# Performance work log

Hardware: AMD Instinct MI355X
Metric: run time of the kernel (lower is better)

The kernel has to match this reference:

```python
import jax, jax.numpy as jnp
import numpy as np

I1, H1, H2, NC = 38, 50, 15, 14

def _lstm(x, w_ih, w_hh, b_ih, b_hh):
    # x: [B, T, I]; weights in torch layout: w_ih [4H, I], w_hh [4H, H]
    # torch gate order: i, f, g, o
    B, T, _ = x.shape
    H = w_hh.shape[1]
    gx = jnp.einsum('bti,gi->btg', x, w_ih) + b_ih + b_hh  # [B, T, 4H]
    gx = jnp.swapaxes(gx, 0, 1)  # [T, B, 4H]

    def step(carry, g_t):
        h, c = carry
        g = g_t + h @ w_hh.T
        i_g, f_g, c_g, o_g = jnp.split(g, 4, axis=-1)
        i_g = jax.nn.sigmoid(i_g)
        f_g = jax.nn.sigmoid(f_g)
        o_g = jax.nn.sigmoid(o_g)
        c = f_g * c + i_g * jnp.tanh(c_g)
        h = o_g * jnp.tanh(c)
        return (h, c), h

    init = (jnp.zeros((B, H), x.dtype), jnp.zeros((B, H), x.dtype))
    _, hs = jax.lax.scan(step, init, gx)  # hs: [T, B, H]
    return jnp.swapaxes(hs, 0, 1)  # [B, T, H]

def setup_inputs() -> dict:
    key = jax.random.key(0)
    ks = jax.random.split(key, 12)
    s1 = 1.0 / np.sqrt(H1)
    s2 = 1.0 / np.sqrt(H2)
    u = lambda k, shape, s: jax.random.uniform(k, shape, jnp.float32, -s, s)
    return {
        'x': jax.random.normal(ks[0], (4096, 256, I1), jnp.float32),
        'w_ih1': u(ks[1], (4 * H1, I1), s1),
        'w_hh1': u(ks[2], (4 * H1, H1), s1),
        'b_ih1': u(ks[3], (4 * H1,), s1),
        'b_hh1': u(ks[4], (4 * H1,), s1),
        'w_ih2': u(ks[5], (4 * H2, H1), s2),
        'w_hh2': u(ks[6], (4 * H2, H2), s2),
        'b_ih2': u(ks[7], (4 * H2,), s2),
        'b_hh2': u(ks[8], (4 * H2,), s2),
        'w_fc': u(ks[9], (NC, H2), s2),
        'b_fc': u(ks[10], (NC,), s2),
    }

def reference(x, w_ih1, w_hh1, b_ih1, b_hh1, w_ih2, w_hh2, b_ih2, b_hh2, w_fc, b_fc):
    out = _lstm(x, w_ih1, w_hh1, b_ih1, b_hh1)          # [B, T, 50]
    # dropout(0.2) is identity in eval mode
    out = _lstm(out, w_ih2, w_hh2, b_ih2, b_hh2)        # [B, T, 15]
    return out[:, -1, :] @ w_fc.T + b_fc                # [B, 14]
```

## Files before the change

kernel.cpp:

```cpp
#include <hip/hip_runtime.h>


typedef _Float16 f16x8 __attribute__((ext_vector_type(8)));
typedef float    f32x4 __attribute__((ext_vector_type(4)));

#if __has_builtin(__builtin_amdgcn_exp2f)
#define DEV_EXP2(x) __builtin_amdgcn_exp2f(x)
#else
#define DEV_EXP2(x) exp2f(x)
#endif
#if __has_builtin(__builtin_amdgcn_rcpf)
#define DEV_RCP(x) __builtin_amdgcn_rcpf(x)
#else
#define DEV_RCP(x) (1.0f/(x))
#endif

#define I1 38
#define H1 50
#define H2 15
#define NC 14
#define TT 256
#define SB 16
#define XS 136
#define NTH 512
#define L2E 2.885390081777927f
#define L1E 1.442695040888963f

#define MF(A,B,C) __builtin_amdgcn_mfma_f32_16x16x32_f16((A),(B),(C),0,0,0)

__device__ __forceinline__ float sigm(float v)  { return DEV_RCP(1.f + DEV_EXP2(-L1E * v)); }
__device__ __forceinline__ float tanh_f(float v){ return 1.f - 2.f * DEV_RCP(1.f + DEV_EXP2(L2E * v)); }

__launch_bounds__(NTH, 1)
__global__ void lstm2_fused(const float* __restrict__ x,
                            const float* __restrict__ w_ih1, const float* __restrict__ w_hh1,
                            const float* __restrict__ b_ih1, const float* __restrict__ b_hh1,
                            const float* __restrict__ w_ih2, const float* __restrict__ w_hh2,
                            const float* __restrict__ b_ih2, const float* __restrict__ b_hh2,
                            const float* __restrict__ w_fc, const float* __restrict__ b_fc,
                            float* __restrict__ out)
{
  __shared__ __align__(16) _Float16 bufA[2][SB][XS];

  const int tid  = threadIdx.x;
  const int wv   = tid >> 6;
  const int lane = tid & 63;
  const int lm   = lane & 15;
  const int lk   = lane >> 4;
  const int blk  = blockIdx.x;
  const float* xblk = x + (size_t)blk * SB * TT * I1;

  for (int i = tid; i < 2*SB*XS; i += NTH) ((_Float16*)bufA)[i] = (_Float16)0.f;

  auto welem = [&](bool il1, bool valid, int u, int g, int k) -> _Float16 {
    float w = 0.f;
    if (valid) {
      if (il1) {
        if (k < I1)                w = w_ih1[(g*H1 + u)*I1 + k];
        else if (k < I1 + H1)      w = w_hh1[(g*H1 + u)*H1 + (k - I1)];
      } else {
        if (k >= I1 && k < I1+H1)             w = w_ih2[(g*H2 + u)*H1 + (k - I1)];
        else if (k >= I1+H1 && k < I1+H1+H2)  w = w_hh2[(g*H2 + u)*H2 + (k - I1 - H1)];
      }
    }
    return (_Float16)w;
  };

  const int t1 = wv + 8;
  const int r0 = wv*16 + lm, u0f = r0 >> 2, g0 = r0 & 3;
  const int r1 = t1*16 + lm, q1 = r1 >> 2, g1 = r1 & 3;
  const bool il1f = (q1 < H1);
  const int  u1f = il1f ? q1 : (q1 - H1);
  const bool w16 = (wv == 0);
  const bool c16 = w16 && (lm < 4);

  f16x8 W0[3], W1[4], W16[3];
  #pragma unroll
  for (int ks = 0; ks < 3; ++ks) {
    f16x8 v;
    #pragma unroll
    for (int e = 0; e < 8; ++e) v[e] = welem(true, true, u0f, g0, ks*32 + lk*8 + e);
    W0[ks] = v;
  }
  #pragma unroll
  for (int ks = 0; ks < 4; ++ks) {
    f16x8 v;
    #pragma unroll
    for (int e = 0; e < 8; ++e) v[e] = welem(il1f, true, u1f, g1, ks*32 + lk*8 + e);
    W1[ks] = v;
  }
  #pragma unroll
  for (int j = 0; j < 3; ++j) {
    f16x8 v;
    #pragma unroll
    for (int e = 0; e < 8; ++e) v[e] = welem(false, c16, 14, lm & 3, (j+1)*32 + lk*8 + e);
    W16[j] = v;
  }

  const int uS0 = 4*wv + lk;
  const int d0  = 38 + uS0;
  const int uS1 = 32 + 4*wv + lk;
  const bool il1u = (uS1 < H1);
  const int  uS1r = il1u ? uS1 : (uS1 - H1);
  const int  d1   = il1u ? (38 + uS1) : (88 + uS1r);
  const bool hasC = w16 && (lk == 0);

  float sb0[4], sb1[4], sbC[4];
  #pragma unroll
  for (int m = 0; m < 4; ++m) {
    sb0[m] = b_ih1[m*H1 + uS0] + b_hh1[m*H1 + uS0];
    sb1[m] = il1u ? (b_ih1[m*H1 + uS1] + b_hh1[m*H1 + uS1])
                  : (b_ih2[m*H2 + uS1r] + b_hh2[m*H2 + uS1r]);
    sbC[m] = b_ih2[m*H2 + 14] + b_hh2[m*H2 + 14];
  }

  const int e1x = tid + 512;
  const bool v1 = (tid < SB*I1 - 512);
  const int s0 = tid / I1,  k0 = tid % I1;
  const int s1 = e1x / I1,  k1 = e1x % I1;
  const int gb0 = s0*TT*I1 + k0, gb1 = v1 ? (s1*TT*I1 + k1) : 0;
  const int lb0 = s0*XS + k0,    lb1 = v1 ? (s1*XS + k1) : 0;

  __syncthreads();
  {
    _Float16* b0 = &bufA[0][0][0];
    b0[lb0] = (_Float16)xblk[gb0];
    if (v1) b0[lb1] = (_Float16)xblk[gb1];
  }
  float xA0 = 0.f, xA1 = 0.f, xB0 = 0.f, xB1 = 0.f;
  xA0 = xblk[gb0 + I1];
  if (v1) xA1 = xblk[gb1 + I1];
  __syncthreads();

  float cS0 = 0.f, cS1 = 0.f, cC = 0.f;

#define STEP(T, XC0, XC1, XN0, XN1) do {                                        \
    _Float16* cur = &bufA[(T) & 1][0][0];                                       \
    _Float16* nxt = &bufA[((T) & 1) ^ 1][0][0];                                 \
    if ((T) + 2 < TT) {                                                         \
      const int go = ((T) + 2) * I1;                                            \
      XN0 = xblk[gb0 + go];                                                     \
      if (v1) XN1 = xblk[gb1 + go];                                             \
    }                                                                           \
    f16x8 a0 = *(const f16x8*)(cur + lm*XS +      lk*8);                        \
    f16x8 a1 = *(const f16x8*)(cur + lm*XS + 32 + lk*8);                        \
    f16x8 a2 = *(const f16x8*)(cur + lm*XS + 64 + lk*8);                        \
    f16x8 a3 = *(const f16x8*)(cur + lm*XS + 96 + lk*8);                        \
    {                                                                           \
      f32x4 acc = (f32x4){sb0[0], sb0[1], sb0[2], sb0[3]};                      \
      acc = MF(W0[0], a0, acc);                                                 \
      acc = MF(W0[1], a1, acc);                                                 \
      acc = MF(W0[2], a2, acc);                                                 \
      if ((T) < TT) {                                                           \
        float ig = sigm(acc[0]), fg = sigm(acc[1]);                             \
        float gg = tanh_f(acc[2]), og = sigm(acc[3]);                           \
        cS0 = fg*cS0 + ig*gg;                                                   \
        nxt[lm*XS + d0] = (_Float16)(og * tanh_f(cS0));                         \
      }                                                                         \
    }                                                                           \
    {                                                                           \
      f32x4 acc = (f32x4){sb1[0], sb1[1], sb1[2], sb1[3]};                      \
      acc = MF(W1[0], a0, acc);                                                 \
      acc = MF(W1[1], a1, acc);                                                 \
      acc = MF(W1[2], a2, acc);                                                 \
      acc = MF(W1[3], a3, acc);                                                 \
      const bool up = il1u ? ((T) < TT) : ((T) >= 1);                           \
      if (up) {                                                                 \
        float ig = sigm(acc[0]), fg = sigm(acc[1]);                             \
        float gg = tanh_f(acc[2]), og = sigm(acc[3]);                           \
        cS1 = fg*cS1 + ig*gg;                                                   \
        nxt[lm*XS + d1] = (_Float16)(og * tanh_f(cS1));                         \
      }                                                                         \
    }                                                                           \
    if (w16) {                                                                  \
      f32x4 acc = (f32x4){sbC[0], sbC[1], sbC[2], sbC[3]};                      \
      acc = MF(W16[0], a1, acc);                                                \
      acc = MF(W16[1], a2, acc);                                                \
      acc = MF(W16[2], a3, acc);                                                \
      if (hasC && (T) >= 1) {                                                   \
        float ig = sigm(acc[0]), fg = sigm(acc[1]);                             \
        float gg = tanh_f(acc[2]), og = sigm(acc[3]);                           \
        cC = fg*cC + ig*gg;                                                     \
        nxt[lm*XS + 102] = (_Float16)(og * tanh_f(cC));                         \
      }                                                                         \
    }                                                                           \
    if ((T) + 1 < TT) {                                                         \
      nxt[lb0] = (_Float16)XC0;                                                 \
      if (v1) nxt[lb1] = (_Float16)XC1;                                         \
    }                                                                           \
    __syncthreads();                                                            \
  } while (0)

  int t = 0;
  for (;;) {
    STEP(t, xA0, xA1, xB0, xB1);
    if (++t > TT) break;
    STEP(t, xB0, xB1, xA0, xA1);
    if (++t > TT) break;
  }
#undef STEP

  if (tid < SB*NC) {
    int s = tid / NC, n = tid % NC;
    float acc = b_fc[n];
    #pragma unroll
    for (int u = 0; u < H2; ++u)
      acc += (float)bufA[1][s][88 + u] * w_fc[n*H2 + u];
    out[((size_t)blk*SB + s)*NC + n] = acc;
  }
}

extern "C" void kernel_launch(void* const* d_in, const int* in_sizes, int n_in,
                              void* d_out, int out_size, void* d_ws, size_t ws_size,
                              hipStream_t stream) {
  (void)n_in; (void)d_ws; (void)ws_size; (void)out_size;
  const float* x     = (const float*)d_in[0];
  const float* w_ih1 = (const float*)d_in[1];
  const float* w_hh1 = (const float*)d_in[2];
  const float* b_ih1 = (const float*)d_in[3];
  const float* b_hh1 = (const float*)d_in[4];
  const float* w_ih2 = (const float*)d_in[5];
  const float* w_hh2 = (const float*)d_in[6];
  const float* b_ih2 = (const float*)d_in[7];
  const float* b_hh2 = (const float*)d_in[8];
  const float* w_fc  = (const float*)d_in[9];
  const float* b_fc  = (const float*)d_in[10];
  float* out = (float*)d_out;

  const int B = in_sizes[0] / (TT * I1);
  dim3 grid(B / SB), block(NTH);
  lstm2_fused<<<grid, block, 0, stream>>>(x, w_ih1, w_hh1, b_ih1, b_hh1,
                                          w_ih2, w_hh2, b_ih2, b_hh2,
                                          w_fc, b_fc, out);
}
```

Before: 163.3 us.

## Stage input timesteps through double-buffered LDS windows with vectorized loads

Replaces the per-step scalar global loads of x, which were prefetched two steps ahead into registers, with float4 loads of 8-timestep windows per sample. The windows are converted to fp16 and staged in a double-buffered shared-memory array. Each step then copies its x slice from LDS into the recurrent input buffer. This cuts the number of global load instructions and makes the accesses coalesced. The trade-off is that the global load latency now lands inside one step out of every eight, and the kernel uses extra shared memory.

```diff
diff --git a/kernel.cpp b/kernel.cpp
--- a/kernel.cpp
+++ b/kernel.cpp
@@ -2,6 +2,7 @@
 
 
 typedef _Float16 f16x8 __attribute__((ext_vector_type(8)));
+typedef _Float16 f16x4 __attribute__((ext_vector_type(4)));
 typedef float    f32x4 __attribute__((ext_vector_type(4)));
 
 #if __has_builtin(__builtin_amdgcn_exp2f)
@@ -23,6 +24,7 @@
 #define SB 16
 #define XS 136
 #define NTH 512
+#define WROW 304
 #define L2E 2.885390081777927f
 #define L1E 1.442695040888963f
 
@@ -41,6 +43,7 @@
                             float* __restrict__ out)
 {
   __shared__ __align__(16) _Float16 bufA[2][SB][XS];
+  __shared__ __align__(16) _Float16 s_win[2][SB][WROW];
 
   const int tid  = threadIdx.x;
   const int wv   = tid >> 6;
@@ -114,91 +117,98 @@
     sbC[m] = b_ih2[m*H2 + 14] + b_hh2[m*H2 + 14];
   }
 
+  auto load_window = [&](int t0, int buf) {
+    #pragma unroll
+    for (int it = 0; it < 3; ++it) {
+      int c = it*NTH + tid;
+      if (c < SB*76) {
+        int s = c / 76, r = c % 76;
+        const float4 v = *(const float4*)(xblk + (size_t)s*(TT*I1) + t0*I1 + 4*r);
+        f16x4 h;
+        h[0] = (_Float16)v.x; h[1] = (_Float16)v.y;
+        h[2] = (_Float16)v.z; h[3] = (_Float16)v.w;
+        *(f16x4*)&s_win[buf][s][4*r] = h;
+      }
+    }
+  };
+
   const int e1x = tid + 512;
   const bool v1 = (tid < SB*I1 - 512);
   const int s0 = tid / I1,  k0 = tid % I1;
   const int s1 = e1x / I1,  k1 = e1x % I1;
-  const int gb0 = s0*TT*I1 + k0, gb1 = v1 ? (s1*TT*I1 + k1) : 0;
-  const int lb0 = s0*XS + k0,    lb1 = v1 ? (s1*XS + k1) : 0;
-
+  const int lb0 = s0*XS + k0, lb1 = v1 ? (s1*XS + k1) : 0;
+
+  load_window(0, 0);
+  load_window(8, 1);
   __syncthreads();
   {
     _Float16* b0 = &bufA[0][0][0];
-    b0[lb0] = (_Float16)xblk[gb0];
-    if (v1) b0[lb1] = (_Float16)xblk[gb1];
-  }
-  float xA0 = 0.f, xA1 = 0.f, xB0 = 0.f, xB1 = 0.f;
-  xA0 = xblk[gb0 + I1];
-  if (v1) xA1 = xblk[gb1 + I1];
+    b0[lb0] = s_win[0][s0][k0];
+    if (v1) b0[lb1] = s_win[0][s1][k1];
+  }
   __syncthreads();
 
   float cS0 = 0.f, cS1 = 0.f, cC = 0.f;
 
-#define STEP(T, XC0, XC1, XN0, XN1) do {                                        \
-    _Float16* cur = &bufA[(T) & 1][0][0];                                       \
-    _Float16* nxt = &bufA[((T) & 1) ^ 1][0][0];                                 \
-    if ((T) + 2 < TT) {                                                         \
-      const int go = ((T) + 2) * I1;                                            \
-      XN0 = xblk[gb0 + go];                                                     \
-      if (v1) XN1 = xblk[gb1 + go];                                             \
-    }                                                                           \
-    f16x8 a0 = *(const f16x8*)(cur + lm*XS +      lk*8);                        \
-    f16x8 a1 = *(const f16x8*)(cur + lm*XS + 32 + lk*8);                        \
-    f16x8 a2 = *(const f16x8*)(cur + lm*XS + 64 + lk*8);                        \
-    f16x8 a3 = *(const f16x8*)(cur + lm*XS + 96 + lk*8);                        \
-    {                                                                           \
-      f32x4 acc = (f32x4){sb0[0], sb0[1], sb0[2], sb0[3]};                      \
-      acc = MF(W0[0], a0, acc);                                                 \
-      acc = MF(W0[1], a1, acc);                                                 \
-      acc = MF(W0[2], a2, acc);                                                 \
-      if ((T) < TT) {                                                           \
-        float ig = sigm(acc[0]), fg = sigm(acc[1]);                             \
-        float gg = tanh_f(acc[2]), og = sigm(acc[3]);                           \
-        cS0 = fg*cS0 + ig*gg;                                                   \
-        nxt[lm*XS + d0] = (_Float16)(og * tanh_f(cS0));                         \
-      }                                                                         \
-    }                                                                           \
-    {                                                                           \
-      f32x4 acc = (f32x4){sb1[0], sb1[1], sb1[2], sb1[3]};                      \
-      acc = MF(W1[0], a0, acc);                                                 \
-      acc = MF(W1[1], a1, acc);                                                 \
-      acc = MF(W1[2], a2, acc);                                                 \
-      acc = MF(W1[3], a3, acc);                                                 \
-      const bool up = il1u ? ((T) < TT) : ((T) >= 1);                           \
-      if (up) {                                                                 \
-        float ig = sigm(acc[0]), fg = sigm(acc[1]);                             \
-        float gg = tanh_f(acc[2]), og = sigm(acc[3]);                           \
-        cS1 = fg*cS1 + ig*gg;                                                   \
-        nxt[lm*XS + d1] = (_Float16)(og * tanh_f(cS1));                         \
-      }                                                                         \
-    }                                                                           \
-    if (w16) {                                                                  \
-      f32x4 acc = (f32x4){sbC[0], sbC[1], sbC[2], sbC[3]};                      \
-      acc = MF(W16[0], a1, acc);                                                \
-      acc = MF(W16[1], a2, acc);                                                \
-      acc = MF(W16[2], a3, acc);                                                \
-      if (hasC && (T) >= 1) {                                                   \
-        float ig = sigm(acc[0]), fg = sigm(acc[1]);                             \
-        float gg = tanh_f(acc[2]), og = sigm(acc[3]);                           \
-        cC = fg*cC + ig*gg;                                                     \
-        nxt[lm*XS + 102] = (_Float16)(og * tanh_f(cC));                         \
-      }                                                                         \
-    }                                                                           \
-    if ((T) + 1 < TT) {                                                         \
-      nxt[lb0] = (_Float16)XC0;                                                 \
-      if (v1) nxt[lb1] = (_Float16)XC1;                                         \
-    }                                                                           \
-    __syncthreads();                                                            \
-  } while (0)
-
-  int t = 0;
-  for (;;) {
-    STEP(t, xA0, xA1, xB0, xB1);
-    if (++t > TT) break;
-    STEP(t, xB0, xB1, xA0, xA1);
-    if (++t > TT) break;
-  }
-#undef STEP
+  for (int t = 0; t <= TT; ++t) {
+    _Float16* cur = &bufA[t & 1][0][0];
+    _Float16* nxt = &bufA[(t & 1) ^ 1][0][0];
+
+    if ((t & 7) == 7 && t + 9 < TT)
+      load_window(t + 9, ((t + 9) >> 3) & 1);
+
+    f16x8 a0 = *(const f16x8*)(cur + lm*XS +      lk*8);
+    f16x8 a1 = *(const f16x8*)(cur + lm*XS + 32 + lk*8);
+    f16x8 a2 = *(const f16x8*)(cur + lm*XS + 64 + lk*8);
+    f16x8 a3 = *(const f16x8*)(cur + lm*XS + 96 + lk*8);
+
+    {
+      f32x4 acc = (f32x4){sb0[0], sb0[1], sb0[2], sb0[3]};
+      acc = MF(W0[0], a0, acc);
+      acc = MF(W0[1], a1, acc);
+      acc = MF(W0[2], a2, acc);
+      if (t < TT) {
+        float ig = sigm(acc[0]), fg = sigm(acc[1]);
+        float gg = tanh_f(acc[2]), og = sigm(acc[3]);
+        cS0 = fg*cS0 + ig*gg;
+        nxt[lm*XS + d0] = (_Float16)(og * tanh_f(cS0));
+      }
+    }
+    {
+      f32x4 acc = (f32x4){sb1[0], sb1[1], sb1[2], sb1[3]};
+      acc = MF(W1[0], a0, acc);
+      acc = MF(W1[1], a1, acc);
+      acc = MF(W1[2], a2, acc);
+      acc = MF(W1[3], a3, acc);
+      const bool up = il1u ? (t < TT) : (t >= 1);
+      if (up) {
+        float ig = sigm(acc[0]), fg = sigm(acc[1]);
+        float gg = tanh_f(acc[2]), og = sigm(acc[3]);
+        cS1 = fg*cS1 + ig*gg;
+        nxt[lm*XS + d1] = (_Float16)(og * tanh_f(cS1));
+      }
+    }
+    if (w16) {
+      f32x4 acc = (f32x4){sbC[0], sbC[1], sbC[2], sbC[3]};
+      acc = MF(W16[0], a1, acc);
+      acc = MF(W16[1], a2, acc);
+      acc = MF(W16[2], a3, acc);
+      if (hasC && t >= 1) {
+        float ig = sigm(acc[0]), fg = sigm(acc[1]);
+        float gg = tanh_f(acc[2]), og = sigm(acc[3]);
+        cC = fg*cC + ig*gg;
+        nxt[lm*XS + 102] = (_Float16)(og * tanh_f(cC));
+      }
+    }
+
+    if (t + 1 < TT) {
+      const int tw = (t + 1) & 7, bw = ((t + 1) >> 3) & 1;
+      nxt[lb0] = s_win[bw][s0][tw*I1 + k0];
+      if (v1) nxt[lb1] = s_win[bw][s1][tw*I1 + k1];
+    }
+
+    __syncthreads();
+  }
 
   if (tid < SB*NC) {
     int s = tid / NC, n = tid % NC;
```

After: 201.8 us. +23.5%, slower.

## Halve sequences per block and fold gate tiles onto four waves

Applied to the files above, without the earlier changes.

Each block now handles 8 sequences with 256 threads instead of 16 with 512. Each of the four waves runs four gate tiles rather than two, and MFMA rows 8-15 duplicate rows 0-7 with their writes masked off. With launch bounds of 2 blocks per CU there are twice as many blocks, which shortens per-step barrier cost and should raise occupancy. In exchange, half of the MFMA work is wasted on duplicated rows and each wave holds more weight registers, which may cap how many waves fit.

```diff
diff --git a/kernel.cpp b/kernel.cpp
--- a/kernel.cpp
+++ b/kernel.cpp
@@ -20,9 +20,9 @@
 #define H2 15
 #define NC 14
 #define TT 256
-#define SB 16
+#define SB 8
 #define XS 136
-#define NTH 512
+#define NTH 256
 #define L2E 2.885390081777927f
 #define L1E 1.442695040888963f
 
@@ -31,7 +31,7 @@
 __device__ __forceinline__ float sigm(float v)  { return DEV_RCP(1.f + DEV_EXP2(-L1E * v)); }
 __device__ __forceinline__ float tanh_f(float v){ return 1.f - 2.f * DEV_RCP(1.f + DEV_EXP2(L2E * v)); }
 
-__launch_bounds__(NTH, 1)
+__launch_bounds__(NTH, 2)
 __global__ void lstm2_fused(const float* __restrict__ x,
                             const float* __restrict__ w_ih1, const float* __restrict__ w_hh1,
                             const float* __restrict__ b_ih1, const float* __restrict__ b_hh1,
@@ -47,6 +47,7 @@
   const int lane = tid & 63;
   const int lm   = lane & 15;
   const int lk   = lane >> 4;
+  const int arow = lm & 7;
   const int blk  = blockIdx.x;
   const float* xblk = x + (size_t)blk * SB * TT * I1;
 
@@ -66,28 +67,37 @@
     return (_Float16)w;
   };
 
-  const int t1 = wv + 8;
-  const int r0 = wv*16 + lm, u0f = r0 >> 2, g0 = r0 & 3;
-  const int r1 = t1*16 + lm, q1 = r1 >> 2, g1 = r1 & 3;
-  const bool il1f = (q1 < H1);
-  const int  u1f = il1f ? q1 : (q1 - H1);
-  const bool w16 = (wv == 0);
+  int   uF[4]; bool il1F[4];
+  #pragma unroll
+  for (int s = 0; s < 4; ++s) {
+    const int r = (wv + 4*s)*16 + lm;
+    const int q = r >> 2;
+    il1F[s] = (q < H1);
+    uF[s]   = il1F[s] ? q : (q - H1);
+  }
+  const int gF = lm & 3;
+  const bool w16 = (wv == 3);
   const bool c16 = w16 && (lm < 4);
 
-  f16x8 W0[3], W1[4], W16[3];
+  f16x8 W0[3], W1[3], W2[3], W3[4], W16[3];
   #pragma unroll
   for (int ks = 0; ks < 3; ++ks) {
-    f16x8 v;
-    #pragma unroll
-    for (int e = 0; e < 8; ++e) v[e] = welem(true, true, u0f, g0, ks*32 + lk*8 + e);
-    W0[ks] = v;
+    f16x8 v0, v1v, v2;
+    #pragma unroll
+    for (int e = 0; e < 8; ++e) {
+      const int k = ks*32 + lk*8 + e;
+      v0[e]  = welem(il1F[0], true, uF[0], gF, k);
+      v1v[e] = welem(il1F[1], true, uF[1], gF, k);
+      v2[e]  = welem(il1F[2], true, uF[2], gF, k);
+    }
+    W0[ks] = v0; W1[ks] = v1v; W2[ks] = v2;
   }
   #pragma unroll
   for (int ks = 0; ks < 4; ++ks) {
     f16x8 v;
     #pragma unroll
-    for (int e = 0; e < 8; ++e) v[e] = welem(il1f, true, u1f, g1, ks*32 + lk*8 + e);
-    W1[ks] = v;
+    for (int e = 0; e < 8; ++e) v[e] = welem(il1F[3], true, uF[3], gF, ks*32 + lk*8 + e);
+    W3[ks] = v;
   }
   #pragma unroll
   for (int j = 0; j < 3; ++j) {
@@ -97,25 +107,26 @@
     W16[j] = v;
   }
 
-  const int uS0 = 4*wv + lk;
-  const int d0  = 38 + uS0;
-  const int uS1 = 32 + 4*wv + lk;
-  const bool il1u = (uS1 < H1);
-  const int  uS1r = il1u ? uS1 : (uS1 - H1);
-  const int  d1   = il1u ? (38 + uS1) : (88 + uS1r);
+  int dU[4]; bool il1U[4];
+  float sb[4][4];
+  #pragma unroll
+  for (int s = 0; s < 4; ++s) {
+    const int u = 4*(wv + 4*s) + lk;
+    il1U[s] = (u < H1);
+    const int ur = il1U[s] ? u : (u - H1);
+    dU[s] = il1U[s] ? (38 + u) : (88 + ur);
+    #pragma unroll
+    for (int m = 0; m < 4; ++m)
+      sb[s][m] = il1U[s] ? (b_ih1[m*H1 + u] + b_hh1[m*H1 + u])
+                         : (b_ih2[m*H2 + ur] + b_hh2[m*H2 + ur]);
+  }
   const bool hasC = w16 && (lk == 0);
-
-  float sb0[4], sb1[4], sbC[4];
-  #pragma unroll
-  for (int m = 0; m < 4; ++m) {
-    sb0[m] = b_ih1[m*H1 + uS0] + b_hh1[m*H1 + uS0];
-    sb1[m] = il1u ? (b_ih1[m*H1 + uS1] + b_hh1[m*H1 + uS1])
-                  : (b_ih2[m*H2 + uS1r] + b_hh2[m*H2 + uS1r]);
-    sbC[m] = b_ih2[m*H2 + 14] + b_hh2[m*H2 + 14];
-  }
-
-  const int e1x = tid + 512;
-  const bool v1 = (tid < SB*I1 - 512);
+  float sbC[4];
+  #pragma unroll
+  for (int m = 0; m < 4; ++m) sbC[m] = b_ih2[m*H2 + 14] + b_hh2[m*H2 + 14];
+
+  const int e1x = tid + 256;
+  const bool v1 = (tid < SB*I1 - 256);
   const int s0 = tid / I1,  k0 = tid % I1;
   const int s1 = e1x / I1,  k1 = e1x % I1;
   const int gb0 = s0*TT*I1 + k0, gb1 = v1 ? (s1*TT*I1 + k1) : 0;
@@ -132,7 +143,17 @@
   if (v1) xA1 = xblk[gb1 + I1];
   __syncthreads();
 
-  float cS0 = 0.f, cS1 = 0.f, cC = 0.f;
+  float cS[4] = {0.f, 0.f, 0.f, 0.f};
+  float cC = 0.f;
+
+  auto upd = [&](const f32x4& acc, float& c, int dcol, bool up, _Float16* nxt) {
+    if (up && lm < SB) {
+      float ig = sigm(acc[0]), fg = sigm(acc[1]);
+      float gg = tanh_f(acc[2]), og = sigm(acc[3]);
+      c = fg * c + ig * gg;
+      nxt[lm*XS + dcol] = (_Float16)(og * tanh_f(c));
+    }
+  };
 
 #define STEP(T, XC0, XC1, XN0, XN1) do {                                        \
     _Float16* cur = &bufA[(T) & 1][0][0];                                       \
@@ -142,46 +163,43 @@
       XN0 = xblk[gb0 + go];                                                     \
       if (v1) XN1 = xblk[gb1 + go];                                             \
     }                                                                           \
-    f16x8 a0 = *(const f16x8*)(cur + lm*XS +      lk*8);                        \
-    f16x8 a1 = *(const f16x8*)(cur + lm*XS + 32 + lk*8);                        \
-    f16x8 a2 = *(const f16x8*)(cur + lm*XS + 64 + lk*8);                        \
-    f16x8 a3 = *(const f16x8*)(cur + lm*XS + 96 + lk*8);                        \
-    {                                                                           \
-      f32x4 acc = (f32x4){sb0[0], sb0[1], sb0[2], sb0[3]};                      \
-      acc = MF(W0[0], a0, acc);                                                 \
-      acc = MF(W0[1], a1, acc);                                                 \
+    f16x8 a0 = *(const f16x8*)(cur + arow*XS +      lk*8);                      \
+    f16x8 a1 = *(const f16x8*)(cur + arow*XS + 32 + lk*8);                      \
+    f16x8 a2 = *(const f16x8*)(cur + arow*XS + 64 + lk*8);                      \
+    f16x8 a3 = *(const f16x8*)(cur + arow*XS + 96 + lk*8);                      \
+    {                                                                           \
+      f32x4 acc = (f32x4){sb[0][0], sb[0][1], sb[0][2], sb[0][3]};              \
+      acc = MF(W0[0], a0, acc); acc = MF(W0[1], a1, acc);                       \
       acc = MF(W0[2], a2, acc);                                                 \
-      if ((T) < TT) {                                                           \
-        float ig = sigm(acc[0]), fg = sigm(acc[1]);                             \
-        float gg = tanh_f(acc[2]), og = sigm(acc[3]);                           \
-        cS0 = fg*cS0 + ig*gg;                                                   \
-        nxt[lm*XS + d0] = (_Float16)(og * tanh_f(cS0));                         \
-      }                                                                         \
-    }                                                                           \
-    {                                                                           \
-      f32x4 acc = (f32x4){sb1[0], sb1[1], sb1[2], sb1[3]};                      \
-      acc = MF(W1[0], a0, acc);                                                 \
-      acc = MF(W1[1], a1, acc);                                                 \
+      upd(acc, cS[0], dU[0], (T) < TT, nxt);                                    \
+    }                                                                           \
+    {                                                                           \
+      f32x4 acc = (f32x4){sb[1][0], sb[1][1], sb[1][2], sb[1][3]};              \
+      acc = MF(W1[0], a0, acc); acc = MF(W1[1], a1, acc);                       \
       acc = MF(W1[2], a2, acc);                                                 \
-      acc = MF(W1[3], a3, acc);                                                 \
-      const bool up = il1u ? ((T) < TT) : ((T) >= 1);                           \
-      if (up) {                                                                 \
-        float ig = sigm(acc[0]), fg = sigm(acc[1]);                             \
-        float gg = tanh_f(acc[2]), og = sigm(acc[3]);                           \
-        cS1 = fg*cS1 + ig*gg;                                                   \
-        nxt[lm*XS + d1] = (_Float16)(og * tanh_f(cS1));                         \
-      }                                                                         \
+      upd(acc, cS[1], dU[1], (T) < TT, nxt);                                    \
+    }                                                                           \
+    {                                                                           \
+      f32x4 acc = (f32x4){sb[2][0], sb[2][1], sb[2][2], sb[2][3]};              \
+      acc = MF(W2[0], a0, acc); acc = MF(W2[1], a1, acc);                       \
+      acc = MF(W2[2], a2, acc);                                                 \
+      upd(acc, cS[2], dU[2], (T) < TT, nxt);                                    \
+    }                                                                           \
+    {                                                                           \
+      f32x4 acc = (f32x4){sb[3][0], sb[3][1], sb[3][2], sb[3][3]};              \
+      acc = MF(W3[0], a0, acc); acc = MF(W3[1], a1, acc);                       \
+      acc = MF(W3[2], a2, acc); acc = MF(W3[3], a3, acc);                       \
+      upd(acc, cS[3], dU[3], il1U[3] ? ((T) < TT) : ((T) >= 1), nxt);           \
     }                                                                           \
     if (w16) {                                                                  \
       f32x4 acc = (f32x4){sbC[0], sbC[1], sbC[2], sbC[3]};                      \
-      acc = MF(W16[0], a1, acc);                                                \
-      acc = MF(W16[1], a2, acc);                                                \
+      acc = MF(W16[0], a1, acc); acc = MF(W16[1], a2, acc);                     \
       acc = MF(W16[2], a3, acc);                                                \
       if (hasC && (T) >= 1) {                                                   \
         float ig = sigm(acc[0]), fg = sigm(acc[1]);                             \
         float gg = tanh_f(acc[2]), og = sigm(acc[3]);                           \
         cC = fg*cC + ig*gg;                                                     \
-        nxt[lm*XS + 102] = (_Float16)(og * tanh_f(cC));                         \
+        if (lm < SB) nxt[lm*XS + 102] = (_Float16)(og * tanh_f(cC));            \
       }                                                                         \
     }                                                                           \
     if ((T) + 1 < TT) {                                                         \
```

After: 267.5 us. +63.8%, slower.

## Halve workgroup to 4 waves, each computing four gate tiles; vectorize x loads

Applied to the files above, without the earlier changes.

The block now runs with 256 threads instead of 512, so each of the 4 waves owns four 16-row MFMA gate tiles rather than two, and the layer-2 cell-14 tile moves to wave 3. Input x loads and f16 stores to LDS are widened to float2/f16x2 pairs, and the loader indexing is changed to match. The goal is cheaper per-timestep __syncthreads barriers and fewer memory instructions. The cost is a longer serial MFMA and transcendental chain per wave on every timestep, plus more weight registers per wave.

```diff
diff --git a/kernel.cpp b/kernel.cpp
--- a/kernel.cpp
+++ b/kernel.cpp
@@ -2,6 +2,7 @@
 
 
 typedef _Float16 f16x8 __attribute__((ext_vector_type(8)));
+typedef _Float16 f16x2 __attribute__((ext_vector_type(2)));
 typedef float    f32x4 __attribute__((ext_vector_type(4)));
 
 #if __has_builtin(__builtin_amdgcn_exp2f)
@@ -22,7 +23,7 @@
 #define TT 256
 #define SB 16
 #define XS 136
-#define NTH 512
+#define NTH 256
 #define L2E 2.885390081777927f
 #define L1E 1.442695040888963f
 
@@ -66,81 +67,101 @@
     return (_Float16)w;
   };
 
-  const int t1 = wv + 8;
-  const int r0 = wv*16 + lm, u0f = r0 >> 2, g0 = r0 & 3;
-  const int r1 = t1*16 + lm, q1 = r1 >> 2, g1 = r1 & 3;
-  const bool il1f = (q1 < H1);
-  const int  u1f = il1f ? q1 : (q1 - H1);
-  const bool w16 = (wv == 0);
-  const bool c16 = w16 && (lm < 4);
-
-  f16x8 W0[3], W1[4], W16[3];
+  auto wfrag = [&](int ts, int ks) -> f16x8 {
+    const int r = ts*16 + lm, q = r >> 2, g = r & 3;
+    const bool il1 = (q < H1);
+    const int u = il1 ? q : (q - H1);
+    f16x8 v;
+    #pragma unroll
+    for (int e = 0; e < 8; ++e) v[e] = welem(il1, true, u, g, ks*32 + lk*8 + e);
+    return v;
+  };
+
+  f16x8 W0[3], W1[3], W2[3], W3[4], W16[3];
   #pragma unroll
   for (int ks = 0; ks < 3; ++ks) {
-    f16x8 v;
-    #pragma unroll
-    for (int e = 0; e < 8; ++e) v[e] = welem(true, true, u0f, g0, ks*32 + lk*8 + e);
-    W0[ks] = v;
-  }
-  #pragma unroll
-  for (int ks = 0; ks < 4; ++ks) {
-    f16x8 v;
-    #pragma unroll
-    for (int e = 0; e < 8; ++e) v[e] = welem(il1f, true, u1f, g1, ks*32 + lk*8 + e);
-    W1[ks] = v;
-  }
+    W0[ks] = wfrag(wv,      ks);
+    W1[ks] = wfrag(wv + 4,  ks);
+    W2[ks] = wfrag(wv + 8,  ks);
+    W3[ks] = wfrag(wv + 12, ks);
+  }
+  W3[3] = wfrag(wv + 12, 3);
   #pragma unroll
   for (int j = 0; j < 3; ++j) {
     f16x8 v;
     #pragma unroll
-    for (int e = 0; e < 8; ++e) v[e] = welem(false, c16, 14, lm & 3, (j+1)*32 + lk*8 + e);
+    for (int e = 0; e < 8; ++e) v[e] = welem(false, lm < 4, 14, lm & 3, (j+1)*32 + lk*8 + e);
     W16[j] = v;
   }
 
-  const int uS0 = 4*wv + lk;
-  const int d0  = 38 + uS0;
-  const int uS1 = 32 + 4*wv + lk;
-  const bool il1u = (uS1 < H1);
-  const int  uS1r = il1u ? uS1 : (uS1 - H1);
-  const int  d1   = il1u ? (38 + uS1) : (88 + uS1r);
-  const bool hasC = w16 && (lk == 0);
-
-  float sb0[4], sb1[4], sbC[4];
+  auto bval = [&](int ts, int m) -> float {
+    const int u = 4*ts + lk;
+    if (u < H1) return b_ih1[m*H1 + u] + b_hh1[m*H1 + u];
+    const int ur = u - H1;
+    return b_ih2[m*H2 + ur] + b_hh2[m*H2 + ur];
+  };
+  float sb0[4], sb1[4], sb2[4], sb3[4], sbC[4];
   #pragma unroll
   for (int m = 0; m < 4; ++m) {
-    sb0[m] = b_ih1[m*H1 + uS0] + b_hh1[m*H1 + uS0];
-    sb1[m] = il1u ? (b_ih1[m*H1 + uS1] + b_hh1[m*H1 + uS1])
-                  : (b_ih2[m*H2 + uS1r] + b_hh2[m*H2 + uS1r]);
+    sb0[m] = bval(wv, m);
+    sb1[m] = bval(wv + 4, m);
+    sb2[m] = bval(wv + 8, m);
+    sb3[m] = bval(wv + 12, m);
     sbC[m] = b_ih2[m*H2 + 14] + b_hh2[m*H2 + 14];
   }
 
-  const int e1x = tid + 512;
-  const bool v1 = (tid < SB*I1 - 512);
-  const int s0 = tid / I1,  k0 = tid % I1;
-  const int s1 = e1x / I1,  k1 = e1x % I1;
-  const int gb0 = s0*TT*I1 + k0, gb1 = v1 ? (s1*TT*I1 + k1) : 0;
-  const int lb0 = s0*XS + k0,    lb1 = v1 ? (s1*XS + k1) : 0;
+  const int d0 = 38 + (4*wv + lk);
+  const int d1 = 38 + (4*(wv+4) + lk);
+  const int d2 = 38 + (4*(wv+8) + lk);
+  const int u3 = 4*(wv+12) + lk;
+  const bool il13 = (u3 < H1);
+  const int d3 = il13 ? (38 + u3) : (88 + (u3 - H1));
+  const bool w16 = (wv == 3);
+
+  const int c1x = tid + 256;
+  const bool v1 = (c1x < SB*19);
+  const int s0 = tid / 19,  q0 = tid % 19;
+  const int s1x = c1x / 19, q1x = c1x % 19;
+  const int gb0 = s0*TT*I1 + 2*q0;
+  const int gb1 = v1 ? (s1x*TT*I1 + 2*q1x) : 0;
+  const int lb0 = s0*XS + 2*q0;
+  const int lb1 = v1 ? (s1x*XS + 2*q1x) : 0;
+
+  auto st2 = [&](_Float16* dst, float2 v) {
+    f16x2 h; h[0] = (_Float16)v.x; h[1] = (_Float16)v.y;
+    *(f16x2*)dst = h;
+  };
 
   __syncthreads();
   {
     _Float16* b0 = &bufA[0][0][0];
-    b0[lb0] = (_Float16)xblk[gb0];
-    if (v1) b0[lb1] = (_Float16)xblk[gb1];
-  }
-  float xA0 = 0.f, xA1 = 0.f, xB0 = 0.f, xB1 = 0.f;
-  xA0 = xblk[gb0 + I1];
-  if (v1) xA1 = xblk[gb1 + I1];
+    st2(b0 + lb0, *(const float2*)(xblk + gb0));
+    if (v1) st2(b0 + lb1, *(const float2*)(xblk + gb1));
+  }
+  float2 xA0v = {0.f, 0.f}, xA1v = {0.f, 0.f};
+  float2 xB0v = {0.f, 0.f}, xB1v = {0.f, 0.f};
+  xA0v = *(const float2*)(xblk + gb0 + I1);
+  if (v1) xA1v = *(const float2*)(xblk + gb1 + I1);
   __syncthreads();
 
-  float cS0 = 0.f, cS1 = 0.f, cC = 0.f;
+  float c0s = 0.f, c1s = 0.f, c2s = 0.f, c3s = 0.f, cC = 0.f;
+
+#define UPD_L1(ACC, CVAR, DCOL, T) do {                                         \
+    if ((T) < TT) {                                                             \
+      float ig = sigm((ACC)[0]), fg = sigm((ACC)[1]);                           \
+      float gg = tanh_f((ACC)[2]), og = sigm((ACC)[3]);                         \
+      CVAR = fg*CVAR + ig*gg;                                                   \
+      nxt[lm*XS + (DCOL)] = (_Float16)(og * tanh_f(CVAR));                      \
+    }                                                                           \
+  } while (0)
 
 #define STEP(T, XC0, XC1, XN0, XN1) do {                                        \
     _Float16* cur = &bufA[(T) & 1][0][0];                                       \
     _Float16* nxt = &bufA[((T) & 1) ^ 1][0][0];                                 \
     if ((T) + 2 < TT) {                                                         \
       const int go = ((T) + 2) * I1;                                            \
-      XN0 = xblk[gb0 + go];                                                     \
-      if (v1) XN1 = xblk[gb1 + go];                                             \
+      XN0 = *(const float2*)(xblk + gb0 + go);                                  \
+      if (v1) XN1 = *(const float2*)(xblk + gb1 + go);                          \
     }                                                                           \
     f16x8 a0 = *(const f16x8*)(cur + lm*XS +      lk*8);                        \
     f16x8 a1 = *(const f16x8*)(cur + lm*XS + 32 + lk*8);                        \
@@ -148,36 +169,39 @@
     f16x8 a3 = *(const f16x8*)(cur + lm*XS + 96 + lk*8);                        \
     {                                                                           \
       f32x4 acc = (f32x4){sb0[0], sb0[1], sb0[2], sb0[3]};                      \
-      acc = MF(W0[0], a0, acc);                                                 \
-      acc = MF(W0[1], a1, acc);                                                 \
+      acc = MF(W0[0], a0, acc); acc = MF(W0[1], a1, acc);                       \
       acc = MF(W0[2], a2, acc);                                                 \
-      if ((T) < TT) {                                                           \
-        float ig = sigm(acc[0]), fg = sigm(acc[1]);                             \
-        float gg = tanh_f(acc[2]), og = sigm(acc[3]);                           \
-        cS0 = fg*cS0 + ig*gg;                                                   \
-        nxt[lm*XS + d0] = (_Float16)(og * tanh_f(cS0));                         \
-      }                                                                         \
+      UPD_L1(acc, c0s, d0, T);                                                  \
     }                                                                           \
     {                                                                           \
       f32x4 acc = (f32x4){sb1[0], sb1[1], sb1[2], sb1[3]};                      \
-      acc = MF(W1[0], a0, acc);                                                 \
-      acc = MF(W1[1], a1, acc);                                                 \
+      acc = MF(W1[0], a0, acc); acc = MF(W1[1], a1, acc);                       \
       acc = MF(W1[2], a2, acc);                                                 \
-      acc = MF(W1[3], a3, acc);                                                 \
-      const bool up = il1u ? ((T) < TT) : ((T) >= 1);                           \
+      UPD_L1(acc, c1s, d1, T);                                                  \
+    }                                                                           \
+    {                                                                           \
+      f32x4 acc = (f32x4){sb2[0], sb2[1], sb2[2], sb2[3]};                      \
+      acc = MF(W2[0], a0, acc); acc = MF(W2[1], a1, acc);                       \
+      acc = MF(W2[2], a2, acc);                                                 \
+      UPD_L1(acc, c2s, d2, T);                                                  \
+    }                                                                           \
+    {                                                                           \
+      f32x4 acc = (f32x4){sb3[0], sb3[1], sb3[2], sb3[3]};                      \
+      acc = MF(W3[0], a0, acc); acc = MF(W3[1], a1, acc);                       \
+      acc = MF(W3[2], a2, acc); acc = MF(W3[3], a3, acc);                       \
+      const bool up = il13 ? ((T) < TT) : ((T) >= 1);                           \
       if (up) {                                                                 \
         float ig = sigm(acc[0]), fg = sigm(acc[1]);                             \
         float gg = tanh_f(acc[2]), og = sigm(acc[3]);                           \
-        cS1 = fg*cS1 + ig*gg;                                                   \
-        nxt[lm*XS + d1] = (_Float16)(og * tanh_f(cS1));                         \
+        c3s = fg*c3s + ig*gg;                                                   \
+        nxt[lm*XS + d3] = (_Float16)(og * tanh_f(c3s));                         \
       }                                                                         \
     }                                                                           \
     if (w16) {                                                                  \
       f32x4 acc = (f32x4){sbC[0], sbC[1], sbC[2], sbC[3]};                      \
-      acc = MF(W16[0], a1, acc);                                                \
-      acc = MF(W16[1], a2, acc);                                                \
+      acc = MF(W16[0], a1, acc); acc = MF(W16[1], a2, acc);                     \
       acc = MF(W16[2], a3, acc);                                                \
-      if (hasC && (T) >= 1) {                                                   \
+      if (lk == 0 && (T) >= 1) {                                                \
         float ig = sigm(acc[0]), fg = sigm(acc[1]);                             \
         float gg = tanh_f(acc[2]), og = sigm(acc[3]);                           \
         cC = fg*cC + ig*gg;                                                     \
@@ -185,20 +209,21 @@
       }                                                                         \
     }                                                                           \
     if ((T) + 1 < TT) {                                                         \
-      nxt[lb0] = (_Float16)XC0;                                                 \
-      if (v1) nxt[lb1] = (_Float16)XC1;                                         \
+      st2(nxt + lb0, XC0);                                                      \
+      if (v1) st2(nxt + lb1, XC1);                                              \
     }                                                                           \
     __syncthreads();                                                            \
   } while (0)
 
   int t = 0;
   for (;;) {
-    STEP(t, xA0, xA1, xB0, xB1);
+    STEP(t, xA0v, xA1v, xB0v, xB1v);
     if (++t > TT) break;
-    STEP(t, xB0, xB1, xA0, xA1);
+    STEP(t, xB0v, xB1v, xA0v, xA1v);
     if (++t > TT) break;
   }
 #undef STEP
+#undef UPD_L1
 
   if (tid < SB*NC) {
     int s = tid / NC, n = tid % NC;
```

New measurement: 211.2 us. +29.3%, slower.
